# Kernel tuning notes

Measured on AMD Instinct MI355X. Metric: run time of the kernel, lower is better.

## Reference

```python
import jax, jax.numpy as jnp
import numpy as np

BATCH, DIM, LAYER_NUM = 16384, 1024, 3

def setup_inputs() -> dict:
    key = jax.random.key(0)
    k1, k2 = jax.random.split(key)
    x = jax.random.normal(k1, (BATCH, DIM), dtype=jnp.float32)
    # glorot_normal for shape (dim, 1): std = sqrt(2/(dim+1))
    kernels = jax.random.normal(k2, (LAYER_NUM, DIM), dtype=jnp.float32) * np.sqrt(2.0 / (DIM + 1)).astype(np.float32)
    bias = jnp.zeros((LAYER_NUM, DIM), dtype=jnp.float32)
    return {"x": x, "kernels": kernels, "bias": bias}

def reference(x, kernels, bias):
    # CrossNet: x_{l+1} = x_0 * (x_l^T w_l) + x_l + b_l
    # The original builds (B, dim, dim) = x_0 x_l^T then contracts with w_l (dim,1);
    # by associativity this equals x_0 * (x_l . w_l) — identical math, O(dim) work.
    x0 = x
    xl = x
    for i in range(kernels.shape[0]):
        s = jnp.einsum('bd,d->b', xl, kernels[i])  # (B,) scalar x_l^T w
        xl = x0 * s[:, None] + xl + bias[i][None, :]
    return xl
```

## Files before the change

kernel.cpp:

```cpp
#include <hip/hip_runtime.h>


#define CN_BATCH 16384
#define CN_DIM   1024
#define CN_LAYERS 3

__global__ __launch_bounds__(256) void crossnet_kernel(
    const float* __restrict__ x,
    const float* __restrict__ kernels,
    const float* __restrict__ bias,
    float* __restrict__ out)
{
    const int wave = threadIdx.x >> 6;
    const int lane = threadIdx.x & 63;
    const int row  = (blockIdx.x << 2) + wave;

    const float* xrow = x + (size_t)row * CN_DIM;

    float4 x0[4], xl[4];
#pragma unroll
    for (int j = 0; j < 4; ++j) {
        x0[j] = *reinterpret_cast<const float4*>(xrow + j * 256 + lane * 4);
        xl[j] = x0[j];
    }

#pragma unroll
    for (int i = 0; i < CN_LAYERS; ++i) {
        const float* krow = kernels + i * CN_DIM;
        const float* brow = bias    + i * CN_DIM;

        float partial = 0.0f;
#pragma unroll
        for (int j = 0; j < 4; ++j) {
            float4 k = *reinterpret_cast<const float4*>(krow + j * 256 + lane * 4);
            partial = fmaf(xl[j].x, k.x, partial);
            partial = fmaf(xl[j].y, k.y, partial);
            partial = fmaf(xl[j].z, k.z, partial);
            partial = fmaf(xl[j].w, k.w, partial);
        }
#pragma unroll
        for (int off = 32; off >= 1; off >>= 1)
            partial += __shfl_xor(partial, off, 64);
        const float s = partial;

#pragma unroll
        for (int j = 0; j < 4; ++j) {
            float4 b = *reinterpret_cast<const float4*>(brow + j * 256 + lane * 4);
            xl[j].x = fmaf(x0[j].x, s, xl[j].x) + b.x;
            xl[j].y = fmaf(x0[j].y, s, xl[j].y) + b.y;
            xl[j].z = fmaf(x0[j].z, s, xl[j].z) + b.z;
            xl[j].w = fmaf(x0[j].w, s, xl[j].w) + b.w;
        }
    }

    float* orow = out + (size_t)row * CN_DIM;
#pragma unroll
    for (int j = 0; j < 4; ++j)
        *reinterpret_cast<float4*>(orow + j * 256 + lane * 4) = xl[j];
}

extern "C" void kernel_launch(void* const* d_in, const int* in_sizes, int n_in,
                              void* d_out, int out_size, void* d_ws, size_t ws_size,
                              hipStream_t stream) {
    const float* x       = (const float*)d_in[0];
    const float* kernels = (const float*)d_in[1];
    const float* bias    = (const float*)d_in[2];
    float* out           = (float*)d_out;

    dim3 grid(CN_BATCH / 4);
    dim3 block(256);
    crossnet_kernel<<<grid, block, 0, stream>>>(x, kernels, bias, out);
}
```

Measured before the change: 28.75 us.

## Collapse three cross layers into closed form and process four rows per wave

Rewrites the layer recurrence algebraically so that x_l stays x0 times a scalar plus a bias sum. All three dot products are then computed against x0 in one pass, and the output is a single fma per element. Each wave now handles four rows, which amortizes the kernel and bias loads and the shuffle reductions, and output uses nontemporal stores. The grid shrinks to a quarter of its former size, so fewer waves are available to hide memory latency. Register pressure also rises from holding 64 floats of x0 per lane.

Result: faster. 26.43 us (-8.1%).

```diff
diff --git a/kernel.cpp b/kernel.cpp
--- a/kernel.cpp
+++ b/kernel.cpp
@@ -3,7 +3,9 @@
 
 #define CN_BATCH 16384
 #define CN_DIM   1024
-#define CN_LAYERS 3
+#define CN_ROWS  4
+
+typedef float f32x4 __attribute__((ext_vector_type(4)));
 
 __global__ __launch_bounds__(256) void crossnet_kernel(
     const float* __restrict__ x,
@@ -13,50 +15,85 @@
 {
     const int wave = threadIdx.x >> 6;
     const int lane = threadIdx.x & 63;
-    const int row  = (blockIdx.x << 2) + wave;
+    const int base = ((blockIdx.x << 2) + wave) * CN_ROWS;
+    const int eoff = lane * 4;
 
-    const float* xrow = x + (size_t)row * CN_DIM;
+    const float* k1 = kernels;
+    const float* k2 = kernels + CN_DIM;
+    const float* k3 = kernels + 2 * CN_DIM;
+    const float* b1 = bias;
+    const float* b2 = bias + CN_DIM;
+    const float* b3 = bias + 2 * CN_DIM;
 
-    float4 x0[4], xl[4];
+    f32x4 x0[CN_ROWS][4];
+#pragma unroll
+    for (int r = 0; r < CN_ROWS; ++r) {
+        const float* xr = x + (size_t)(base + r) * CN_DIM;
+#pragma unroll
+        for (int j = 0; j < 4; ++j)
+            x0[r][j] = *reinterpret_cast<const f32x4*>(xr + j * 256 + eoff);
+    }
+
+    float a1[CN_ROWS], a2[CN_ROWS], a3[CN_ROWS];
+#pragma unroll
+    for (int r = 0; r < CN_ROWS; ++r) { a1[r] = 0.f; a2[r] = 0.f; a3[r] = 0.f; }
+    float c2 = 0.f, c3 = 0.f;
+    f32x4 Bs[4];
+
 #pragma unroll
     for (int j = 0; j < 4; ++j) {
-        x0[j] = *reinterpret_cast<const float4*>(xrow + j * 256 + lane * 4);
-        xl[j] = x0[j];
+        f32x4 vk1 = *reinterpret_cast<const f32x4*>(k1 + j * 256 + eoff);
+        f32x4 vk2 = *reinterpret_cast<const f32x4*>(k2 + j * 256 + eoff);
+        f32x4 vk3 = *reinterpret_cast<const f32x4*>(k3 + j * 256 + eoff);
+        f32x4 vb1 = *reinterpret_cast<const f32x4*>(b1 + j * 256 + eoff);
+        f32x4 vb2 = *reinterpret_cast<const f32x4*>(b2 + j * 256 + eoff);
+        f32x4 vb3 = *reinterpret_cast<const f32x4*>(b3 + j * 256 + eoff);
+        f32x4 b12 = vb1 + vb2;
+        Bs[j] = b12 + vb3;
+#pragma unroll
+        for (int c = 0; c < 4; ++c) {
+#pragma unroll
+            for (int r = 0; r < CN_ROWS; ++r) {
+                a1[r] = fmaf(x0[r][j][c], vk1[c], a1[r]);
+                a2[r] = fmaf(x0[r][j][c], vk2[c], a2[r]);
+                a3[r] = fmaf(x0[r][j][c], vk3[c], a3[r]);
+            }
+            c2 = fmaf(vb1[c], vk2[c], c2);
+            c3 = fmaf(b12[c], vk3[c], c3);
+        }
     }
 
 #pragma unroll
-    for (int i = 0; i < CN_LAYERS; ++i) {
-        const float* krow = kernels + i * CN_DIM;
-        const float* brow = bias    + i * CN_DIM;
+    for (int o = 32; o >= 1; o >>= 1) {
+#pragma unroll
+        for (int r = 0; r < CN_ROWS; ++r) {
+            a1[r] += __shfl_xor(a1[r], o, 64);
+            a2[r] += __shfl_xor(a2[r], o, 64);
+            a3[r] += __shfl_xor(a3[r], o, 64);
+        }
+        c2 += __shfl_xor(c2, o, 64);
+        c3 += __shfl_xor(c3, o, 64);
+    }
 
-        float partial = 0.0f;
+#pragma unroll
+    for (int r = 0; r < CN_ROWS; ++r) {
+        const float t1 = 1.0f + a1[r];
+        const float s2 = fmaf(t1, a2[r], c2);
+        const float t2 = t1 + s2;
+        const float s3 = fmaf(t2, a3[r], c3);
+        const float t3 = t2 + s3;
+
+        float* orow = out + (size_t)(base + r) * CN_DIM;
 #pragma unroll
         for (int j = 0; j < 4; ++j) {
-            float4 k = *reinterpret_cast<const float4*>(krow + j * 256 + lane * 4);
-            partial = fmaf(xl[j].x, k.x, partial);
-            partial = fmaf(xl[j].y, k.y, partial);
-            partial = fmaf(xl[j].z, k.z, partial);
-            partial = fmaf(xl[j].w, k.w, partial);
-        }
+            f32x4 o;
 #pragma unroll
-        for (int off = 32; off >= 1; off >>= 1)
-            partial += __shfl_xor(partial, off, 64);
-        const float s = partial;
-
-#pragma unroll
-        for (int j = 0; j < 4; ++j) {
-            float4 b = *reinterpret_cast<const float4*>(brow + j * 256 + lane * 4);
-            xl[j].x = fmaf(x0[j].x, s, xl[j].x) + b.x;
-            xl[j].y = fmaf(x0[j].y, s, xl[j].y) + b.y;
-            xl[j].z = fmaf(x0[j].z, s, xl[j].z) + b.z;
-            xl[j].w = fmaf(x0[j].w, s, xl[j].w) + b.w;
+            for (int c = 0; c < 4; ++c)
+                o[c] = fmaf(x0[r][j][c], t3, Bs[j][c]);
+            __builtin_nontemporal_store(o,
+                reinterpret_cast<f32x4*>(orow + j * 256 + eoff));
         }
     }
-
-    float* orow = out + (size_t)row * CN_DIM;
-#pragma unroll
-    for (int j = 0; j < 4; ++j)
-        *reinterpret_cast<float4*>(orow + j * 256 + lane * 4) = xl[j];
 }
 
 extern "C" void kernel_launch(void* const* d_in, const int* in_sizes, int n_in,
@@ -67,7 +104,7 @@
     const float* bias    = (const float*)d_in[2];
     float* out           = (float*)d_out;
 
-    dim3 grid(CN_BATCH / 4);
+    dim3 grid(CN_BATCH / 16);
     dim3 block(256);
     crossnet_kernel<<<grid, block, 0, stream>>>(x, kernels, bias, out);
 }
```
